# Kernel tuning notes

Measured on AMD Instinct MI355X. Metric: run time of the kernel, lower is better.

Reference implementation:

```python
import jax, jax.numpy as jnp
import numpy as np

HIDDEN = 1024
B, S = 4, 2048


def setup_inputs() -> dict:
    key = jax.random.key(0)
    ks = jax.random.split(key, 9)
    scale = 1.0 / np.sqrt(HIDDEN)
    mk = lambda k: (jax.random.normal(k, (HIDDEN, HIDDEN), dtype=jnp.float32) * scale)
    return {
        "x": jax.random.normal(ks[0], (B, S, HIDDEN), dtype=jnp.float32),
        "Wq": mk(ks[1]), "bq": jnp.zeros((HIDDEN,), jnp.float32),
        "Wk": mk(ks[2]), "bk": jnp.zeros((HIDDEN,), jnp.float32),
        "Wv": mk(ks[3]), "bv": jnp.zeros((HIDDEN,), jnp.float32),
        "Wo": mk(ks[4]), "bo": jnp.zeros((HIDDEN,), jnp.float32),
    }


def reference(x, Wq, bq, Wk, bk, Wv, bv, Wo, bo):
    # Single-head attention over the full hidden dim (num_heads unused in source).
    # Linear(H,H): y = x @ W^T + b ; weights stored [out,in] torch-style.
    q = jnp.einsum("bsh,oh->bso", x, Wq) + bq  # [B,S,H]
    k = jnp.einsum("bsh,oh->bso", x, Wk) + bk
    v = jnp.einsum("bsh,oh->bso", x, Wv) + bv
    scores = jnp.einsum("bqh,bkh->bqk", q, k) / jnp.sqrt(jnp.float32(HIDDEN))
    attn = jax.nn.softmax(scores, axis=-1)  # dropout rate is 0.0 (eval-equivalent)
    ctx = jnp.einsum("bqk,bkh->bqh", attn, v)
    return jnp.einsum("bsh,oh->bso", ctx, Wo) + bo
```

## Files before the change

### kernel.cpp

```cpp
#include <hip/hip_runtime.h>

#define HID 1024
#define SEQ 2048
#define NB 4
#define BS 8192

typedef __attribute__((ext_vector_type(8))) short short8;
typedef __attribute__((ext_vector_type(8))) unsigned short ushort8;
typedef __attribute__((ext_vector_type(4))) float f32x4;

__device__ __forceinline__ float bf2f(unsigned short u) {
  unsigned int x = ((unsigned int)u) << 16;
  return __builtin_bit_cast(float, x);
}
__device__ __forceinline__ unsigned short f2bf(float f) {
  unsigned int x = __builtin_bit_cast(unsigned int, f);
  x = x + 0x7fffu + ((x >> 16) & 1u);
  return (unsigned short)(x >> 16);
}

#define GLOAD16(g, l)                                                          \
  __builtin_amdgcn_global_load_lds(                                            \
      (const __attribute__((address_space(1))) unsigned int*)(g),              \
      (__attribute__((address_space(3))) unsigned int*)(l), 16, 0, 0)

__global__ void cast_f32_to_bf16(const float* __restrict__ in,
                                 unsigned short* __restrict__ out, int n) {
  int i = (blockIdx.x * 256 + threadIdx.x) * 8;
  if (i >= n) return;
  f32x4 a = *(const f32x4*)(in + i);
  f32x4 b = *(const f32x4*)(in + i + 4);
  ushort8 o;
  o[0] = f2bf(a[0]); o[1] = f2bf(a[1]); o[2] = f2bf(a[2]); o[3] = f2bf(a[3]);
  o[4] = f2bf(b[0]); o[5] = f2bf(b[1]); o[6] = f2bf(b[2]); o[7] = f2bf(b[3]);
  *(ushort8*)(out + i) = o;
}

__global__ __launch_bounds__(256) void transpose_cast(
    const float* __restrict__ in, unsigned short* __restrict__ out) {
  __shared__ float t[32][33];
  const int bx = blockIdx.x * 32, by = blockIdx.y * 32;
  const int tx = threadIdx.x & 31, ty = threadIdx.x >> 5;
#pragma unroll
  for (int i = 0; i < 4; ++i)
    t[ty + i * 8][tx] = in[(by + ty + i * 8) * 1024 + bx + tx];
  __syncthreads();
#pragma unroll
  for (int i = 0; i < 4; ++i)
    out[(bx + ty + i * 8) * 1024 + by + tx] = f2bf(t[tx][ty + i * 8]);
}

__global__ __launch_bounds__(256) void bias_fuse(const float* __restrict__ Wo,
                                                 const float* __restrict__ bv,
                                                 const float* __restrict__ bo,
                                                 float* __restrict__ bp) {
  const int row = blockIdx.x * 4 + (threadIdx.x >> 6);
  const int lane = threadIdx.x & 63;
  float s = 0.f;
  for (int k = lane; k < 1024; k += 64) s += Wo[row * 1024 + k] * bv[k];
#pragma unroll
  for (int off = 32; off >= 1; off >>= 1) s += __shfl_xor(s, off, 64);
  if (lane == 0) bp[row] = s + bo[row];
}

template <int OUT_F32, int BIAS_MODE, int EPI>
__global__ __launch_bounds__(256, 2) void gemm_w(
    const unsigned short* __restrict__ A, const unsigned short* __restrict__ B,
    void* __restrict__ Cv, const float* __restrict__ bias,
    const float* __restrict__ bias2, float* __restrict__ Srow, int K, int lda,
    int ldb, int ldc, long long bsA, long long bsB, long long bsC,
    float alpha) {
  __shared__ unsigned short lA[2][256 * 32];
  __shared__ unsigned short lB[2][128 * 32];

  const int tid = threadIdx.x;
  const int lane = tid & 63, wid = tid >> 6;
  const int fr = lane & 15, fq = lane >> 4;
  const int wm = wid >> 1, wn = wid & 1;

  const int nx = gridDim.x;
  const int nwg = nx * gridDim.y;
  int f = blockIdx.y * nx + blockIdx.x;
  f = (f & 7) * (nwg >> 3) + (f >> 3);
  const int bx = f % nx, by = f / nx;
  const int bz = blockIdx.z;

  const unsigned short* Ag = A + bz * bsA + (long long)by * 256 * lda;
  const unsigned short* Bg = B + bz * bsB + (long long)bx * 128 * ldb;
  const int NT = K >> 5;

  const int srow = tid >> 2;
  const int scol = 8 * ((tid & 3) ^ ((tid >> 3) & 3));
  const int lbase = wid * 512;

  auto stageA = [&](int t, int b) {
#pragma unroll
    for (int c = 0; c < 4; ++c)
      GLOAD16(Ag + (long long)(c * 64 + srow) * lda + t * 32 + scol,
              &lA[b][c * 2048 + lbase]);
  };
  auto stageB = [&](int t, int b) {
#pragma unroll
    for (int c = 0; c < 2; ++c)
      GLOAD16(Bg + (long long)(c * 64 + srow) * ldb + t * 32 + scol,
              &lB[b][c * 2048 + lbase]);
  };

  const int xm = ((fr >> 1) & 3) << 3;

  f32x4 acc[8][4] = {};

  auto compute = [&](const unsigned short* pa, const unsigned short* pb) {
    short8 av[8], bw[4];
#pragma unroll
    for (int i = 0; i < 8; ++i)
      av[i] = *(const short8*)(pa +
                               (((wm * 128 + i * 16 + fr) * 32 + fq * 8) ^ xm));
#pragma unroll
    for (int n = 0; n < 4; ++n)
      bw[n] = *(const short8*)(pb +
                               (((wn * 64 + n * 16 + fr) * 32 + fq * 8) ^ xm));
    asm volatile("s_waitcnt lgkmcnt(0)" ::: "memory");
    __builtin_amdgcn_sched_barrier(0);
#pragma unroll
    for (int i = 0; i < 8; ++i)
#pragma unroll
      for (int n = 0; n < 4; ++n)
        acc[i][n] = __builtin_amdgcn_mfma_f32_16x16x32_bf16(av[i], bw[n],
                                                            acc[i][n], 0, 0, 0);
  };

  stageA(0, 0);
  stageB(0, 0);
  __syncthreads();

  for (int t = 0; t < NT; t += 2) {
    stageA(t + 1, 1);
    stageB(t + 1, 1);
    compute(lA[0], lB[0]);
    __syncthreads();
    if (t + 2 < NT) {
      stageA(t + 2, 0);
      stageB(t + 2, 0);
    }
    compute(lA[1], lB[1]);
    __syncthreads();
  }

  const long long cb0 = (long long)bz * bsC;
  float* sredf = (float*)lA;
#pragma unroll
  for (int i = 0; i < 8; ++i)
#pragma unroll
    for (int j = 0; j < 4; ++j) {
      const int row = wm * 128 + i * 16 + fq * 4 + j;
      float inv = 1.0f;
      if (EPI == 2) inv = 1.0f / Srow[(long long)bz * SEQ + by * 256 + row];
      float rps = 0.0f;
#pragma unroll
      for (int n = 0; n < 4; ++n) {
        const int col = bx * 128 + wn * 64 + n * 16 + fr;
        float v = acc[i][n][j] * alpha;
        if (EPI == 1) { v = __expf(v); rps += v; }
        if (EPI == 2) v *= inv;
        if (BIAS_MODE == 1) v += bias[col];
        if (BIAS_MODE == 3) v += (col < 1024) ? bias[col] : bias2[col - 1024];
        const long long idx = cb0 + (long long)(by * 256 + row) * ldc + col;
        if (OUT_F32)
          ((float*)Cv)[idx] = v;
        else
          ((unsigned short*)Cv)[idx] = f2bf(v);
      }
      if (EPI == 1) {
        rps += __shfl_xor(rps, 1, 64);
        rps += __shfl_xor(rps, 2, 64);
        rps += __shfl_xor(rps, 4, 64);
        rps += __shfl_xor(rps, 8, 64);
        if (fr == 0) sredf[row * 2 + wn] = rps;
      }
    }
  if (EPI == 1) {
    __syncthreads();
    if (tid < 256) {
      const float s2 = sredf[tid * 2] + sredf[tid * 2 + 1];
      atomicAdd(Srow + (long long)bz * SEQ + by * 256 + tid, s2);
    }
  }
}

extern "C" void kernel_launch(void* const* d_in, const int* in_sizes, int n_in,
                              void* d_out, int out_size, void* d_ws,
                              size_t ws_size, hipStream_t stream) {
  (void)in_sizes; (void)n_in; (void)out_size; (void)ws_size;
  const float* x = (const float*)d_in[0];
  const float* Wq = (const float*)d_in[1];
  const float* bq = (const float*)d_in[2];
  const float* Wk = (const float*)d_in[3];
  const float* bk = (const float*)d_in[4];
  const float* Wv = (const float*)d_in[5];
  const float* bv = (const float*)d_in[6];
  const float* Wo = (const float*)d_in[7];
  const float* bo = (const float*)d_in[8];
  float* out = (float*)d_out;

  char* ws = (char*)d_ws;
  unsigned short* xbf  = (unsigned short*)(ws + 0);
  unsigned short* wqk  = (unsigned short*)(ws + 16777216);
  unsigned short* wobf = (unsigned short*)(ws + 20971520);
  unsigned short* wvT  = (unsigned short*)(ws + 23068672);
  unsigned short* wov  = (unsigned short*)(ws + 25165824);
  float*          bpr  = (float*)        (ws + 27262976);
  float*          Srow = (float*)        (ws + 28311552);
  unsigned short* VWoT = (unsigned short*)(ws + 33554432);
  unsigned short* QKb  = (unsigned short*)(ws + 50331648);
  unsigned short* P    = (unsigned short*)(ws + 83886080);

  cast_f32_to_bf16<<<4096, 256, 0, stream>>>(x, xbf, BS * HID);
  cast_f32_to_bf16<<<512, 256, 0, stream>>>(Wq, wqk, HID * HID);
  cast_f32_to_bf16<<<512, 256, 0, stream>>>(Wk, wqk + HID * HID, HID * HID);
  cast_f32_to_bf16<<<512, 256, 0, stream>>>(Wo, wobf, HID * HID);
  transpose_cast<<<dim3(32, 32), 256, 0, stream>>>(Wv, wvT);
  bias_fuse<<<256, 256, 0, stream>>>(Wo, bv, bo, bpr);
  hipMemsetAsync(Srow, 0, NB * SEQ * sizeof(float), stream);

  gemm_w<0, 0, 0><<<dim3(8, 4, 1), 256, 0, stream>>>(
      wobf, wvT, wov, nullptr, nullptr, nullptr, HID, HID, HID, HID, 0, 0, 0,
      1.0f);
  gemm_w<0, 0, 0><<<dim3(64, 4, 1), 256, 0, stream>>>(
      wov, xbf, VWoT, nullptr, nullptr, nullptr, HID, HID, HID, BS, 0, 0, 0,
      1.0f);
  gemm_w<0, 3, 0><<<dim3(16, 32, 1), 256, 0, stream>>>(
      xbf, wqk, QKb, bq, bk, nullptr, HID, HID, HID, 2048, 0, 0, 0, 1.0f);
  gemm_w<0, 0, 1><<<dim3(16, 8, NB), 256, 0, stream>>>(
      QKb, QKb + 1024, P, nullptr, nullptr, Srow, HID, 2048, 2048, SEQ,
      (long long)SEQ * 2048, (long long)SEQ * 2048, (long long)SEQ * SEQ,
      0.03125f);
  gemm_w<1, 1, 2><<<dim3(8, 8, NB), 256, 0, stream>>>(
      P, VWoT, out, bpr, nullptr, Srow, SEQ, SEQ, BS, HID,
      (long long)SEQ * SEQ, (long long)SEQ, (long long)SEQ * HID, 1.0f);
}
```

Measured before the change: 237.6 us.

## Rewrite GEMM as 512-thread, BK=64 kernel with 256x256 tiles for QK

Replaces the 256-thread GEMM with a 512-thread variant that stages K in chunks of 64 with an 8-way XOR swizzle, single barrier per K step, and optional 256-wide N tiles for the QK projection and score GEMMs. It also raises MFMA wave priority during compute. The aim is more reuse per LDS load and fewer barriers per K, at the cost of more LDS (up to 128 KB per block) and possibly lower occupancy or fewer blocks for small grids.

Measured after the change: 215.4 us. 1.1x faster.

```diff
diff --git a/kernel.cpp b/kernel.cpp
--- a/kernel.cpp
+++ b/kernel.cpp
@@ -63,20 +63,27 @@
   if (lane == 0) bp[row] = s + bo[row];
 }
 
-template <int OUT_F32, int BIAS_MODE, int EPI>
-__global__ __launch_bounds__(256, 2) void gemm_w(
+template <int BN, int OUT_F32, int BIAS_MODE, int EPI>
+__global__ __launch_bounds__(512, 2) void gemm2p(
     const unsigned short* __restrict__ A, const unsigned short* __restrict__ B,
     void* __restrict__ Cv, const float* __restrict__ bias,
     const float* __restrict__ bias2, float* __restrict__ Srow, int K, int lda,
     int ldb, int ldc, long long bsA, long long bsB, long long bsC,
     float alpha) {
-  __shared__ unsigned short lA[2][256 * 32];
-  __shared__ unsigned short lB[2][128 * 32];
+  static_assert(BN == 256 || BN == 128, "BN");
+  constexpr int WMW = (BN == 256) ? 2 : 4;
+  constexpr int WNW = 8 / WMW;
+  constexpr int MI = (256 / WMW) / 16;
+  constexpr int GB = BN / 64;
+  constexpr int WROWS = 256 / WMW;
+
+  __shared__ unsigned short lA[2][256 * 64];
+  __shared__ unsigned short lB[2][BN * 64];
 
   const int tid = threadIdx.x;
   const int lane = tid & 63, wid = tid >> 6;
   const int fr = lane & 15, fq = lane >> 4;
-  const int wm = wid >> 1, wn = wid & 1;
+  const int wm = wid / WNW, wn = wid % WNW;
 
   const int nx = gridDim.x;
   const int nwg = nx * gridDim.y;
@@ -86,85 +93,82 @@
   const int bz = blockIdx.z;
 
   const unsigned short* Ag = A + bz * bsA + (long long)by * 256 * lda;
-  const unsigned short* Bg = B + bz * bsB + (long long)bx * 128 * ldb;
-  const int NT = K >> 5;
-
-  const int srow = tid >> 2;
-  const int scol = 8 * ((tid & 3) ^ ((tid >> 3) & 3));
-  const int lbase = wid * 512;
-
-  auto stageA = [&](int t, int b) {
+  const unsigned short* Bg = B + bz * bsB + (long long)bx * BN * ldb;
+  const int NT = K >> 6;
+
+  const int srow = tid >> 3;
+  const int gcol = 8 * ((tid & 7) ^ ((tid >> 3) & 7));
+  const int ldst = wid * 512;
+
+  auto stage = [&](int t) {
+    const int b = t & 1;
 #pragma unroll
     for (int c = 0; c < 4; ++c)
-      GLOAD16(Ag + (long long)(c * 64 + srow) * lda + t * 32 + scol,
-              &lA[b][c * 2048 + lbase]);
+      GLOAD16(Ag + (long long)(c * 64 + srow) * lda + t * 64 + gcol,
+              &lA[b][c * 4096 + ldst]);
+#pragma unroll
+    for (int c = 0; c < GB; ++c)
+      GLOAD16(Bg + (long long)(c * 64 + srow) * ldb + t * 64 + gcol,
+              &lB[b][c * 4096 + ldst]);
   };
-  auto stageB = [&](int t, int b) {
-#pragma unroll
-    for (int c = 0; c < 2; ++c)
-      GLOAD16(Bg + (long long)(c * 64 + srow) * ldb + t * 32 + scol,
-              &lB[b][c * 2048 + lbase]);
-  };
-
-  const int xm = ((fr >> 1) & 3) << 3;
-
-  f32x4 acc[8][4] = {};
-
-  auto compute = [&](const unsigned short* pa, const unsigned short* pb) {
-    short8 av[8], bw[4];
-#pragma unroll
-    for (int i = 0; i < 8; ++i)
-      av[i] = *(const short8*)(pa +
-                               (((wm * 128 + i * 16 + fr) * 32 + fq * 8) ^ xm));
+
+  const int rxor = fr & 7;
+  f32x4 acc[MI][4] = {};
+
+  auto phase = [&](const unsigned short* pa, const unsigned short* pb,
+                   int kk) {
+    short8 av[MI], bw[4];
+    const int slot = ((kk << 2) | fq) ^ rxor;
+#pragma unroll
+    for (int i = 0; i < MI; ++i)
+      av[i] = *(const short8*)(pa + (wm * WROWS + i * 16 + fr) * 64 + slot * 8);
 #pragma unroll
     for (int n = 0; n < 4; ++n)
-      bw[n] = *(const short8*)(pb +
-                               (((wn * 64 + n * 16 + fr) * 32 + fq * 8) ^ xm));
+      bw[n] = *(const short8*)(pb + (wn * 64 + n * 16 + fr) * 64 + slot * 8);
     asm volatile("s_waitcnt lgkmcnt(0)" ::: "memory");
     __builtin_amdgcn_sched_barrier(0);
-#pragma unroll
-    for (int i = 0; i < 8; ++i)
+    __builtin_amdgcn_s_setprio(1);
+#pragma unroll
+    for (int i = 0; i < MI; ++i)
 #pragma unroll
       for (int n = 0; n < 4; ++n)
         acc[i][n] = __builtin_amdgcn_mfma_f32_16x16x32_bf16(av[i], bw[n],
                                                             acc[i][n], 0, 0, 0);
+    __builtin_amdgcn_s_setprio(0);
   };
 
-  stageA(0, 0);
-  stageB(0, 0);
-  __syncthreads();
-
-  for (int t = 0; t < NT; t += 2) {
-    stageA(t + 1, 1);
-    stageB(t + 1, 1);
-    compute(lA[0], lB[0]);
-    __syncthreads();
-    if (t + 2 < NT) {
-      stageA(t + 2, 0);
-      stageB(t + 2, 0);
-    }
-    compute(lA[1], lB[1]);
-    __syncthreads();
+  stage(0);
+  asm volatile("s_waitcnt vmcnt(0)" ::: "memory");
+  __builtin_amdgcn_s_barrier();
+
+  for (int t = 0; t < NT; ++t) {
+    if (t + 1 < NT) stage(t + 1);
+    const unsigned short* pa = lA[t & 1];
+    const unsigned short* pb = lB[t & 1];
+    phase(pa, pb, 0);
+    phase(pa, pb, 1);
+    asm volatile("s_waitcnt vmcnt(0)" ::: "memory");
+    __builtin_amdgcn_s_barrier();
   }
 
   const long long cb0 = (long long)bz * bsC;
   float* sredf = (float*)lA;
 #pragma unroll
-  for (int i = 0; i < 8; ++i)
+  for (int i = 0; i < MI; ++i)
 #pragma unroll
     for (int j = 0; j < 4; ++j) {
-      const int row = wm * 128 + i * 16 + fq * 4 + j;
+      const int row = wm * WROWS + i * 16 + fq * 4 + j;
       float inv = 1.0f;
       if (EPI == 2) inv = 1.0f / Srow[(long long)bz * SEQ + by * 256 + row];
       float rps = 0.0f;
 #pragma unroll
       for (int n = 0; n < 4; ++n) {
-        const int col = bx * 128 + wn * 64 + n * 16 + fr;
+        const int col = bx * BN + wn * 64 + n * 16 + fr;
         float v = acc[i][n][j] * alpha;
-        if (EPI == 1) { v = __expf(v); rps += v; }
         if (EPI == 2) v *= inv;
         if (BIAS_MODE == 1) v += bias[col];
         if (BIAS_MODE == 3) v += (col < 1024) ? bias[col] : bias2[col - 1024];
+        if (EPI == 1) { v = __expf(v); rps += v; }
         const long long idx = cb0 + (long long)(by * 256 + row) * ldc + col;
         if (OUT_F32)
           ((float*)Cv)[idx] = v;
@@ -176,14 +180,16 @@
         rps += __shfl_xor(rps, 2, 64);
         rps += __shfl_xor(rps, 4, 64);
         rps += __shfl_xor(rps, 8, 64);
-        if (fr == 0) sredf[row * 2 + wn] = rps;
+        if (fr == 0) sredf[row * WNW + wn] = rps;
       }
     }
   if (EPI == 1) {
     __syncthreads();
     if (tid < 256) {
-      const float s2 = sredf[tid * 2] + sredf[tid * 2 + 1];
-      atomicAdd(Srow + (long long)bz * SEQ + by * 256 + tid, s2);
+      float s = 0.f;
+#pragma unroll
+      for (int w = 0; w < WNW; ++w) s += sredf[tid * WNW + w];
+      atomicAdd(Srow + (long long)bz * SEQ + by * 256 + tid, s);
     }
   }
 }
@@ -223,19 +229,19 @@
   bias_fuse<<<256, 256, 0, stream>>>(Wo, bv, bo, bpr);
   hipMemsetAsync(Srow, 0, NB * SEQ * sizeof(float), stream);
 
-  gemm_w<0, 0, 0><<<dim3(8, 4, 1), 256, 0, stream>>>(
+  gemm2p<128, 0, 0, 0><<<dim3(8, 4, 1), 512, 0, stream>>>(
       wobf, wvT, wov, nullptr, nullptr, nullptr, HID, HID, HID, HID, 0, 0, 0,
       1.0f);
-  gemm_w<0, 0, 0><<<dim3(64, 4, 1), 256, 0, stream>>>(
+  gemm2p<128, 0, 0, 0><<<dim3(64, 4, 1), 512, 0, stream>>>(
       wov, xbf, VWoT, nullptr, nullptr, nullptr, HID, HID, HID, BS, 0, 0, 0,
       1.0f);
-  gemm_w<0, 3, 0><<<dim3(16, 32, 1), 256, 0, stream>>>(
+  gemm2p<256, 0, 3, 0><<<dim3(8, 32, 1), 512, 0, stream>>>(
       xbf, wqk, QKb, bq, bk, nullptr, HID, HID, HID, 2048, 0, 0, 0, 1.0f);
-  gemm_w<0, 0, 1><<<dim3(16, 8, NB), 256, 0, stream>>>(
+  gemm2p<256, 0, 0, 1><<<dim3(8, 8, NB), 512, 0, stream>>>(
       QKb, QKb + 1024, P, nullptr, nullptr, Srow, HID, 2048, 2048, SEQ,
       (long long)SEQ * 2048, (long long)SEQ * 2048, (long long)SEQ * SEQ,
       0.03125f);
-  gemm_w<1, 1, 2><<<dim3(8, 8, NB), 256, 0, stream>>>(
+  gemm2p<128, 1, 1, 2><<<dim3(8, 8, NB), 512, 0, stream>>>(
       P, VWoT, out, bpr, nullptr, Srow, SEQ, SEQ, BS, HID,
       (long long)SEQ * SEQ, (long long)SEQ, (long long)SEQ * HID, 1.0f);
 }
```

## Split GEMM workgroup across 8 waves with per-tile barrier and MFMA priority

Applied to the files above, without the earlier changes.

The GEMM kernel moves from 4 to 8 wavefronts per 256x128 tile. Each wave now computes a 64x64 sub-tile, which halves accumulator registers per thread, and launch bounds target 4 blocks per SM. The two-tile unrolled double buffer becomes a single-step loop that prefetches the next K-slice, waits with vmcnt before each barrier, and raises wave priority around the MFMA block. More waves should hide latency better, at the cost of more barriers and more LDS fragment reads per MFMA.

Result: faster. 231.0 us (-2.8%).

```diff
diff --git a/kernel.cpp b/kernel.cpp
--- a/kernel.cpp
+++ b/kernel.cpp
@@ -64,7 +64,7 @@
 }
 
 template <int OUT_F32, int BIAS_MODE, int EPI>
-__global__ __launch_bounds__(256, 2) void gemm_w(
+__global__ __launch_bounds__(512, 4) void gemm_s(
     const unsigned short* __restrict__ A, const unsigned short* __restrict__ B,
     void* __restrict__ Cv, const float* __restrict__ bias,
     const float* __restrict__ bias2, float* __restrict__ Srow, int K, int lda,
@@ -91,69 +91,58 @@
 
   const int srow = tid >> 2;
   const int scol = 8 * ((tid & 3) ^ ((tid >> 3) & 3));
-  const int lbase = wid * 512;
-
-  auto stageA = [&](int t, int b) {
-#pragma unroll
-    for (int c = 0; c < 4; ++c)
-      GLOAD16(Ag + (long long)(c * 64 + srow) * lda + t * 32 + scol,
-              &lA[b][c * 2048 + lbase]);
+  const int ldst = wid * 512;
+
+  auto stage = [&](int t) {
+    const int b = t & 1;
+    GLOAD16(Ag + (long long)srow * lda + t * 32 + scol, &lA[b][ldst]);
+    GLOAD16(Ag + (long long)(128 + srow) * lda + t * 32 + scol,
+            &lA[b][4096 + ldst]);
+    GLOAD16(Bg + (long long)srow * ldb + t * 32 + scol, &lB[b][ldst]);
   };
-  auto stageB = [&](int t, int b) {
-#pragma unroll
-    for (int c = 0; c < 2; ++c)
-      GLOAD16(Bg + (long long)(c * 64 + srow) * ldb + t * 32 + scol,
-              &lB[b][c * 2048 + lbase]);
-  };
 
   const int xm = ((fr >> 1) & 3) << 3;
 
-  f32x4 acc[8][4] = {};
-
-  auto compute = [&](const unsigned short* pa, const unsigned short* pb) {
-    short8 av[8], bw[4];
-#pragma unroll
-    for (int i = 0; i < 8; ++i)
+  f32x4 acc[4][4] = {};
+
+  stage(0);
+  asm volatile("s_waitcnt vmcnt(0)" ::: "memory");
+  __builtin_amdgcn_s_barrier();
+
+  for (int t = 0; t < NT; ++t) {
+    if (t + 1 < NT) stage(t + 1);
+    const unsigned short* pa = lA[t & 1];
+    const unsigned short* pb = lB[t & 1];
+    short8 av[4], bw[4];
+#pragma unroll
+    for (int i = 0; i < 4; ++i)
       av[i] = *(const short8*)(pa +
-                               (((wm * 128 + i * 16 + fr) * 32 + fq * 8) ^ xm));
+                               (((wm * 64 + i * 16 + fr) * 32 + fq * 8) ^ xm));
 #pragma unroll
     for (int n = 0; n < 4; ++n)
       bw[n] = *(const short8*)(pb +
                                (((wn * 64 + n * 16 + fr) * 32 + fq * 8) ^ xm));
     asm volatile("s_waitcnt lgkmcnt(0)" ::: "memory");
     __builtin_amdgcn_sched_barrier(0);
-#pragma unroll
-    for (int i = 0; i < 8; ++i)
+    __builtin_amdgcn_s_setprio(1);
+#pragma unroll
+    for (int i = 0; i < 4; ++i)
 #pragma unroll
       for (int n = 0; n < 4; ++n)
         acc[i][n] = __builtin_amdgcn_mfma_f32_16x16x32_bf16(av[i], bw[n],
                                                             acc[i][n], 0, 0, 0);
-  };
-
-  stageA(0, 0);
-  stageB(0, 0);
-  __syncthreads();
-
-  for (int t = 0; t < NT; t += 2) {
-    stageA(t + 1, 1);
-    stageB(t + 1, 1);
-    compute(lA[0], lB[0]);
-    __syncthreads();
-    if (t + 2 < NT) {
-      stageA(t + 2, 0);
-      stageB(t + 2, 0);
-    }
-    compute(lA[1], lB[1]);
-    __syncthreads();
+    __builtin_amdgcn_s_setprio(0);
+    asm volatile("s_waitcnt vmcnt(0)" ::: "memory");
+    __builtin_amdgcn_s_barrier();
   }
 
   const long long cb0 = (long long)bz * bsC;
   float* sredf = (float*)lA;
 #pragma unroll
-  for (int i = 0; i < 8; ++i)
+  for (int i = 0; i < 4; ++i)
 #pragma unroll
     for (int j = 0; j < 4; ++j) {
-      const int row = wm * 128 + i * 16 + fq * 4 + j;
+      const int row = wm * 64 + i * 16 + fq * 4 + j;
       float inv = 1.0f;
       if (EPI == 2) inv = 1.0f / Srow[(long long)bz * SEQ + by * 256 + row];
       float rps = 0.0f;
@@ -223,19 +212,19 @@
   bias_fuse<<<256, 256, 0, stream>>>(Wo, bv, bo, bpr);
   hipMemsetAsync(Srow, 0, NB * SEQ * sizeof(float), stream);
 
-  gemm_w<0, 0, 0><<<dim3(8, 4, 1), 256, 0, stream>>>(
+  gemm_s<0, 0, 0><<<dim3(8, 4, 1), 512, 0, stream>>>(
       wobf, wvT, wov, nullptr, nullptr, nullptr, HID, HID, HID, HID, 0, 0, 0,
       1.0f);
-  gemm_w<0, 0, 0><<<dim3(64, 4, 1), 256, 0, stream>>>(
+  gemm_s<0, 0, 0><<<dim3(64, 4, 1), 512, 0, stream>>>(
       wov, xbf, VWoT, nullptr, nullptr, nullptr, HID, HID, HID, BS, 0, 0, 0,
       1.0f);
-  gemm_w<0, 3, 0><<<dim3(16, 32, 1), 256, 0, stream>>>(
+  gemm_s<0, 3, 0><<<dim3(16, 32, 1), 512, 0, stream>>>(
       xbf, wqk, QKb, bq, bk, nullptr, HID, HID, HID, 2048, 0, 0, 0, 1.0f);
-  gemm_w<0, 0, 1><<<dim3(16, 8, NB), 256, 0, stream>>>(
+  gemm_s<0, 0, 1><<<dim3(16, 8, NB), 512, 0, stream>>>(
       QKb, QKb + 1024, P, nullptr, nullptr, Srow, HID, 2048, 2048, SEQ,
       (long long)SEQ * 2048, (long long)SEQ * 2048, (long long)SEQ * SEQ,
       0.03125f);
-  gemm_w<1, 1, 2><<<dim3(8, 8, NB), 256, 0, stream>>>(
+  gemm_s<1, 1, 2><<<dim3(8, 8, NB), 512, 0, stream>>>(
       P, VWoT, out, bpr, nullptr, Srow, SEQ, SEQ, BS, HID,
       (long long)SEQ * SEQ, (long long)SEQ, (long long)SEQ * HID, 1.0f);
 }
```
